# Performance work log

Measured on AMD Instinct MI355X. Metric: run time of the kernel, lower is better.

## Reference

```python
import math
import jax, jax.numpy as jnp
from jax import lax
import numpy as np

D_MODEL = 2048
N_HEADS = 16
HEAD_DIM = 128
INNER = N_HEADS * HEAD_DIM  # 2048
KCONV = 4
B, N = 2, 2048


def setup_inputs() -> dict:
    key = jax.random.key(0)
    ks = jax.random.split(key, 7)
    x = jax.random.normal(ks[0], (B, N, D_MODEL), dtype=jnp.float32)
    W_qkv = jax.random.normal(ks[1], (3 * INNER, D_MODEL), dtype=jnp.float32) * 0.02
    conv_w = jax.random.normal(ks[2], (3 * INNER, KCONV), dtype=jnp.float32) * 0.2
    W_ab = jax.random.normal(ks[3], (2 * N_HEADS, D_MODEL), dtype=jnp.float32) * 0.02
    # ab_proj bias init: first H filled with log(0.98/0.02), rest zero
    b_ab = jnp.concatenate([
        jnp.full((N_HEADS,), math.log(0.98 / 0.02), dtype=jnp.float32),
        jnp.zeros((N_HEADS,), dtype=jnp.float32),
    ])
    W_g = jax.random.normal(ks[4], (INNER, D_MODEL), dtype=jnp.float32) * 0.02
    W_o = jax.random.normal(ks[5], (D_MODEL, INNER), dtype=jnp.float32) * 0.02
    return {"x": x, "W_qkv": W_qkv, "conv_w": conv_w, "W_ab": W_ab,
            "b_ab": b_ab, "W_g": W_g, "W_o": W_o}


def _l2_normalize(t, eps=1e-12):
    # torch F.normalize: x / max(||x||_2, eps)
    nrm = jnp.sqrt(jnp.sum(t * t, axis=-1, keepdims=True))
    return t / jnp.maximum(nrm, eps)


def _short_conv(z, conv_w):
    # depthwise causal conv1d + SiLU (FLA-style ShortConvolution, no bias)
    # z: (B, N, C), conv_w: (C, K)
    C, K = conv_w.shape
    zc = jnp.transpose(z, (0, 2, 1))  # (B, C, N)
    kern = conv_w[:, None, :]          # (C, 1, K) -> OIH
    out = lax.conv_general_dilated(
        zc, kern, window_strides=(1,), padding=[(K - 1, 0)],
        dimension_numbers=("NCH", "OIH", "NCH"), feature_group_count=C)
    return jax.nn.silu(jnp.transpose(out, (0, 2, 1)))  # (B, N, C)


def reference(x, W_qkv, conv_w, W_ab, b_ab, W_g, W_o):
    Bq, Nq, _ = x.shape
    H = b_ab.shape[0] // 2
    inner = W_g.shape[0]
    D = inner // H

    qkv = jnp.einsum("bnd,ed->bne", x, W_qkv)            # (B, N, 3*inner)
    qkv = _short_conv(qkv, conv_w)
    q, k, v = jnp.split(qkv, 3, axis=-1)
    to_heads = lambda t: t.reshape(Bq, Nq, H, D).transpose(0, 2, 1, 3)  # (B,H,N,D)
    q, k, v = to_heads(q), to_heads(k), to_heads(v)
    q = _l2_normalize(q)
    k = _l2_normalize(k)

    ab = jnp.einsum("bnd,ed->bne", x, W_ab) + b_ab        # (B, N, 2H)
    alpha = jax.nn.sigmoid(ab[..., :H]).transpose(0, 2, 1)  # (B, H, N)
    beta = jax.nn.sigmoid(ab[..., H:]).transpose(0, 2, 1)   # (B, H, N)

    # gated delta rule recurrence:
    #   S_t = a_t * S_{t-1} + b_t * (v_t - a_t * S_{t-1} k_t) k_t^T
    #   o_t = S_t q_t
    # time-major xs for scan
    q_s = q.transpose(2, 0, 1, 3)   # (N, B, H, D)
    k_s = k.transpose(2, 0, 1, 3)
    v_s = v.transpose(2, 0, 1, 3)
    a_s = alpha.transpose(2, 0, 1)  # (N, B, H)
    b_s = beta.transpose(2, 0, 1)

    S0 = jnp.zeros((Bq, H, D, D), dtype=x.dtype)

    def step(S, inp):
        q_t, k_t, v_t, a_t, b_t = inp
        Sk = jnp.einsum("bhde,bhe->bhd", S, k_t)
        u = b_t[..., None] * (v_t - a_t[..., None] * Sk)
        S = a_t[..., None, None] * S + u[..., :, None] * k_t[..., None, :]
        o = jnp.einsum("bhde,bhe->bhd", S, q_t)
        return S, o

    _, o = lax.scan(step, S0, (q_s, k_s, v_s, a_s, b_s))  # o: (N, B, H, D)
    out = o.transpose(1, 0, 2, 3).reshape(Bq, Nq, inner)

    g = jax.nn.silu(jnp.einsum("bnd,ed->bne", x, W_g))
    out = out * g
    y = jnp.einsum("bne,de->bnd", out, W_o)
    return y
```

## Files before the change

### kernel.cpp

```cpp
#include <hip/hip_runtime.h>
#include <math.h>
#include <stddef.h>

#define B_ 2
#define N_ 2048
#define DM 2048
#define H_ 16
#define HD 128
#define INNER 2048
#define TRIPLE 6144
#define M_ (B_ * N_)
#define T_ 32
#define NCHK (N_ / T_)

typedef __bf16 bf16x8 __attribute__((ext_vector_type(8)));
typedef float  f32x4v __attribute__((ext_vector_type(4)));
typedef __attribute__((address_space(1))) const void gvoid;
typedef __attribute__((address_space(3))) void lvoid;

__device__ __forceinline__ float sig_(float x) { return 1.0f / (1.0f + __expf(-x)); }

__device__ __forceinline__ unsigned short f2bf(float f) {
    unsigned u = __float_as_uint(f);
    u += 0x7FFFu + ((u >> 16) & 1u);
    return (unsigned short)(u >> 16);
}
__device__ __forceinline__ float bf2f(unsigned short h) {
    return __uint_as_float((unsigned)h << 16);
}
__device__ __forceinline__ void unpack8(uint4 r, float* f) {
    f[0] = __uint_as_float(r.x << 16); f[1] = __uint_as_float(r.x & 0xffff0000u);
    f[2] = __uint_as_float(r.y << 16); f[3] = __uint_as_float(r.y & 0xffff0000u);
    f[4] = __uint_as_float(r.z << 16); f[5] = __uint_as_float(r.z & 0xffff0000u);
    f[6] = __uint_as_float(r.w << 16); f[7] = __uint_as_float(r.w & 0xffff0000u);
}

__device__ __forceinline__ void lds_barrier() {
    asm volatile("" ::: "memory");
    __builtin_amdgcn_s_waitcnt(0xC07F);
    __builtin_amdgcn_s_barrier();
    asm volatile("" ::: "memory");
}

__device__ __forceinline__ void bar() {
    asm volatile("" ::: "memory");
    __builtin_amdgcn_s_barrier();
    asm volatile("" ::: "memory");
}

__global__ __launch_bounds__(256) void cast_bf16(
    const float* __restrict__ in, unsigned short* __restrict__ out, int n)
{
    int i = (blockIdx.x * 256 + threadIdx.x) * 4;
    if (i < n) {
        float4 v = *(const float4*)(in + i);
        out[i + 0] = f2bf(v.x); out[i + 1] = f2bf(v.y);
        out[i + 2] = f2bf(v.z); out[i + 3] = f2bf(v.w);
    }
}

__global__ __launch_bounds__(256) void cast_hilo(
    const float* __restrict__ in, unsigned short* __restrict__ hi,
    unsigned short* __restrict__ lo, int n)
{
    int i = (blockIdx.x * 256 + threadIdx.x) * 4;
    if (i < n) {
        float4 v = *(const float4*)(in + i);
        ushort4 h, l;
        h.x = f2bf(v.x); l.x = f2bf(v.x - bf2f(h.x));
        h.y = f2bf(v.y); l.y = f2bf(v.y - bf2f(h.y));
        h.z = f2bf(v.z); l.z = f2bf(v.z - bf2f(h.z));
        h.w = f2bf(v.w); l.w = f2bf(v.w - bf2f(h.w));
        *(ushort4*)(hi + i) = h;
        *(ushort4*)(lo + i) = l;
    }
}

__global__ __launch_bounds__(512) void gemm_fused256(
    const unsigned short* __restrict__ A, const unsigned short* __restrict__ Bw,
    unsigned short* __restrict__ outQ, float* __restrict__ outG,
    int M, int NQ, int NG, int K)
{
    __shared__ unsigned short As[2][256 * 64];
    __shared__ unsigned short Bs[2][256 * 64];

    const int tid = threadIdx.x;
    const int w   = tid >> 6;
    const int l   = tid & 63;
    const int wm  = w >> 2;
    const int wn  = w & 3;
    const int lr  = l & 15;
    const int kg  = l >> 4;

    const int bid = blockIdx.x;
    const int swz = (bid & 7) * 64 + (bid >> 3);
    const int by  = swz & 15;
    const int bx  = swz >> 4;
    const int row0 = by * 256;
    const int col0 = bx * 256;

    const int srow = w * 8 + (l >> 3);
    const int schk = ((l & 7) ^ (l >> 3)) * 8;
    const unsigned short* Ath = A  + (size_t)(row0 + srow) * K + schk;
    const unsigned short* Bth = Bw + (size_t)(col0 + srow) * K + schk;

    const int fsw0 = ((0 + kg) ^ (lr & 7)) * 8;
    const int fsw1 = ((4 + kg) ^ (lr & 7)) * 8;
    const int arb  = wm * 64 + lr;
    const int brb  = wn * 32 + lr;

    f32x4v acc[2][2][4][2];
#pragma unroll
    for (int a0 = 0; a0 < 2; ++a0)
#pragma unroll
        for (int a1 = 0; a1 < 2; ++a1)
#pragma unroll
            for (int a2 = 0; a2 < 4; ++a2)
#pragma unroll
                for (int a3 = 0; a3 < 2; ++a3)
                    acc[a0][a1][a2][a3] = (f32x4v){0.f, 0.f, 0.f, 0.f};

#define STAGE_A(b, hb, kt) do {                                                  \
        const unsigned short* g_ = Ath + (size_t)((hb) * 128) * K + (kt) * 64;   \
        unsigned short* d_ = &As[b][((hb) * 128 + w * 8) * 64];                  \
        __builtin_amdgcn_global_load_lds((gvoid*)g_, (lvoid*)d_, 16, 0, 0);      \
        __builtin_amdgcn_global_load_lds((gvoid*)(g_ + (size_t)64 * K),          \
                                         (lvoid*)(d_ + 64 * 64), 16, 0, 0);      \
    } while (0)
#define STAGE_B(b, hb, kt) do {                                                  \
        const unsigned short* g_ = Bth + (size_t)((hb) * 128) * K + (kt) * 64;   \
        unsigned short* d_ = &Bs[b][((hb) * 128 + w * 8) * 64];                  \
        __builtin_amdgcn_global_load_lds((gvoid*)g_, (lvoid*)d_, 16, 0, 0);      \
        __builtin_amdgcn_global_load_lds((gvoid*)(g_ + (size_t)64 * K),          \
                                         (lvoid*)(d_ + 64 * 64), 16, 0, 0);      \
    } while (0)

#define RD_A(DST, BASE, HOFF)                                        \
    _Pragma("unroll")                                                \
    for (int m_ = 0; m_ < 4; ++m_) {                                 \
        const int r_ = ((HOFF) + arb + m_ * 16) * 64;                \
        DST[m_][0] = *(const bf16x8*)((BASE) + r_ + fsw0);           \
        DST[m_][1] = *(const bf16x8*)((BASE) + r_ + fsw1);           \
    }
#define RD_B(DST, BASE, HOFF)                                        \
    _Pragma("unroll")                                                \
    for (int n_ = 0; n_ < 2; ++n_) {                                 \
        const int r_ = ((HOFF) + brb + n_ * 16) * 64;                \
        DST[n_][0] = *(const bf16x8*)((BASE) + r_ + fsw0);           \
        DST[n_][1] = *(const bf16x8*)((BASE) + r_ + fsw1);           \
    }
#define Q_MFMA(MH, NH, AF, BF)                                               \
    __builtin_amdgcn_s_setprio(1);                                           \
    _Pragma("unroll")                                                        \
    for (int m_ = 0; m_ < 4; ++m_)                                           \
        _Pragma("unroll")                                                    \
        for (int n_ = 0; n_ < 2; ++n_) {                                     \
            acc[MH][NH][m_][n_] = __builtin_amdgcn_mfma_f32_16x16x32_bf16(   \
                AF[m_][0], BF[n_][0], acc[MH][NH][m_][n_], 0, 0, 0);         \
            acc[MH][NH][m_][n_] = __builtin_amdgcn_mfma_f32_16x16x32_bf16(   \
                AF[m_][1], BF[n_][1], acc[MH][NH][m_][n_], 0, 0, 0);         \
        }                                                                    \
    __builtin_amdgcn_s_setprio(0);

    const int KT = K >> 6;

    STAGE_A(0, 0, 0); STAGE_B(0, 0, 0); STAGE_A(0, 1, 0); STAGE_B(0, 1, 0);
    STAGE_A(1, 0, 1); STAGE_B(1, 1, 1);
    asm volatile("s_waitcnt vmcnt(4)" ::: "memory");
    bar();

    bf16x8 aF[4][2];
    bf16x8 aG[4][2];
    bf16x8 bF0[2][2];
    bf16x8 bF1[2][2];

#pragma unroll 2
    for (int kt = 0; kt < KT; ++kt) {
        const unsigned short* Ab = As[kt & 1];
        const unsigned short* Bb = Bs[kt & 1];
        const int nb = (kt + 1) & 1;

        RD_A(aF, Ab, 0);
        RD_B(bF0, Bb, 0);
        if (kt + 1 < KT) STAGE_B(nb, 0, kt + 1);
        bar();

        Q_MFMA(0, 0, aF, bF0);
        RD_B(bF1, Bb, 128);
        if (kt + 1 < KT) STAGE_A(nb, 1, kt + 1);
        bar();

        Q_MFMA(0, 1, aF, bF1);
        RD_A(aG, Ab, 128);
        if (kt + 2 < KT) STAGE_A(kt & 1, 0, kt + 2);
        bar();

        Q_MFMA(1, 1, aG, bF1);
        if (kt + 2 < KT) STAGE_B(kt & 1, 1, kt + 2);
        if (kt < KT - 2)       { asm volatile("s_waitcnt vmcnt(4)" ::: "memory"); }
        else if (kt == KT - 2) { asm volatile("s_waitcnt vmcnt(0)" ::: "memory"); }
        bar();
        Q_MFMA(1, 0, aG, bF0);
    }
#undef STAGE_A
#undef STAGE_B
#undef RD_A
#undef RD_B
#undef Q_MFMA

    const bool isG = (col0 >= NQ);
#pragma unroll
    for (int mh = 0; mh < 2; ++mh)
#pragma unroll
    for (int m = 0; m < 4; ++m) {
        const int rbase = row0 + mh * 128 + wm * 64 + m * 16 + kg * 4;
#pragma unroll
        for (int nh = 0; nh < 2; ++nh)
#pragma unroll
        for (int n = 0; n < 2; ++n) {
            const int c = col0 + nh * 128 + wn * 32 + n * 16 + lr;
#pragma unroll
            for (int j = 0; j < 4; ++j) {
                float v = acc[mh][nh][m][n][j];
                const size_t r = (size_t)(rbase + j);
                if (!isG) {
                    outQ[r * NQ + c] = f2bf(v);
                } else {
                    v = v * sig_(v);
                    outG[r * NG + (c - NQ)] = v;
                }
            }
        }
    }
}

__global__ __launch_bounds__(256) void gemm_bf16f(
    const unsigned short* __restrict__ A, const unsigned short* __restrict__ Bw,
    float* __restrict__ C, int M, int N, int K)
{
    __shared__ unsigned short As[128 * 32];
    __shared__ unsigned short Bs[128 * 32];
    const int tid  = threadIdx.x;
    const int w    = tid >> 6;
    const int l    = tid & 63;
    const int row0 = blockIdx.y * 128;
    const int col0 = blockIdx.x * 128;

    const int sr = tid >> 2;
    const int sc = (tid & 3) * 8;
    const unsigned short* Ag0 = A  + (size_t)(row0 + sr) * K + sc;
    const unsigned short* Ag1 = A  + (size_t)(row0 + 64 + sr) * K + sc;
    const unsigned short* Bg0 = Bw + (size_t)(col0 + sr) * K + sc;
    const unsigned short* Bg1 = Bw + (size_t)(col0 + 64 + sr) * K + sc;
    unsigned short* AsW0 = As + w * 512;
    unsigned short* AsW1 = As + 2048 + w * 512;
    unsigned short* BsW0 = Bs + w * 512;
    unsigned short* BsW1 = Bs + 2048 + w * 512;

    f32x4v acc[4][4];
#pragma unroll
    for (int i = 0; i < 4; ++i)
#pragma unroll
        for (int j = 0; j < 4; ++j) acc[i][j] = (f32x4v){0.f, 0.f, 0.f, 0.f};

    const int m0 = (w >> 1) * 64;
    const int n0 = (w & 1) * 64;
    const int lr = l & 15;
    const int lk = (l >> 4) * 8;

    for (int k0 = 0; k0 < K; k0 += 32) {
        __syncthreads();
        __builtin_amdgcn_global_load_lds((gvoid*)(Ag0 + k0), (lvoid*)AsW0, 16, 0, 0);
        __builtin_amdgcn_global_load_lds((gvoid*)(Ag1 + k0), (lvoid*)AsW1, 16, 0, 0);
        __builtin_amdgcn_global_load_lds((gvoid*)(Bg0 + k0), (lvoid*)BsW0, 16, 0, 0);
        __builtin_amdgcn_global_load_lds((gvoid*)(Bg1 + k0), (lvoid*)BsW1, 16, 0, 0);
        __syncthreads();

        bf16x8 af[4], bfr[4];
#pragma unroll
        for (int i = 0; i < 4; ++i) {
            af[i]  = *(const bf16x8*)&As[(m0 + i * 16 + lr) * 32 + lk];
            bfr[i] = *(const bf16x8*)&Bs[(n0 + i * 16 + lr) * 32 + lk];
        }
#pragma unroll
        for (int mi = 0; mi < 4; ++mi)
#pragma unroll
            for (int ni = 0; ni < 4; ++ni)
                acc[mi][ni] = __builtin_amdgcn_mfma_f32_16x16x32_bf16(
                    af[mi], bfr[ni], acc[mi][ni], 0, 0, 0);
    }

#pragma unroll
    for (int mi = 0; mi < 4; ++mi)
#pragma unroll
        for (int j = 0; j < 4; ++j) {
            int r = row0 + m0 + mi * 16 + (l >> 4) * 4 + j;
#pragma unroll
            for (int ni = 0; ni < 4; ++ni) {
                int c = col0 + n0 + ni * 16 + lr;
                C[(size_t)r * N + c] = acc[mi][ni][j];
            }
        }
}

__global__ __launch_bounds__(256) void gemm_ab(
    const unsigned short* __restrict__ xhi, const unsigned short* __restrict__ xlo,
    const unsigned short* __restrict__ wh, const unsigned short* __restrict__ wl,
    const float* __restrict__ b_ab, float* __restrict__ absig)
{
    __shared__ float sums[4][16][32];
    const int tid = threadIdx.x;
    const int w = tid >> 6, lane = tid & 63;
    const int lr = lane & 15, lk8 = (lane >> 4) * 8, lrow4 = (lane >> 4) * 4;
    const int row = blockIdx.x * 16 + lr;
    const int kw  = w * (DM / 4);

    f32x4v acc[2];
    acc[0] = (f32x4v){0.f,0.f,0.f,0.f};
    acc[1] = (f32x4v){0.f,0.f,0.f,0.f};
    const unsigned short* Ah = xhi + (size_t)row * DM + kw;
    const unsigned short* Al = xlo + (size_t)row * DM + kw;

    for (int k0 = 0; k0 < DM / 4; k0 += 32) {
        bf16x8 ah = *(const bf16x8*)(Ah + k0 + lk8);
        bf16x8 al = *(const bf16x8*)(Al + k0 + lk8);
#pragma unroll
        for (int nt = 0; nt < 2; ++nt) {
            bf16x8 whf = *(const bf16x8*)(wh + (size_t)(nt * 16 + lr) * DM + kw + k0 + lk8);
            bf16x8 wlf = *(const bf16x8*)(wl + (size_t)(nt * 16 + lr) * DM + kw + k0 + lk8);
            acc[nt] = __builtin_amdgcn_mfma_f32_16x16x32_bf16(ah, whf, acc[nt], 0, 0, 0);
            acc[nt] = __builtin_amdgcn_mfma_f32_16x16x32_bf16(ah, wlf, acc[nt], 0, 0, 0);
            acc[nt] = __builtin_amdgcn_mfma_f32_16x16x32_bf16(al, whf, acc[nt], 0, 0, 0);
        }
    }

#pragma unroll
    for (int nt = 0; nt < 2; ++nt)
#pragma unroll
        for (int j = 0; j < 4; ++j)
            sums[w][lrow4 + j][nt * 16 + lr] = acc[nt][j];
    __syncthreads();

    for (int e = tid; e < 512; e += 256) {
        const int r = e >> 5, c = e & 31;
        float s = sums[0][r][c] + sums[1][r][c] + sums[2][r][c] + sums[3][r][c];
        absig[(size_t)(blockIdx.x * 16 + r) * 32 + c] = sig_(s + b_ab[c]);
    }
}

__global__ __launch_bounds__(256) void conv_silu_norm(
    const unsigned short* __restrict__ qkv, const float* __restrict__ conv_w,
    unsigned short* __restrict__ outb)
{
    __shared__ float buf[TRIPLE];
    __shared__ float scales[32];
    const int bn = blockIdx.x;
    const int n = bn & (N_ - 1);
    const int tid = threadIdx.x;
    const unsigned short* base = qkv + (size_t)bn * TRIPLE;

#pragma unroll
    for (int it = 0; it < 3; ++it) {
        const int c8 = (tid + it * 256) * 8;
        float cw[32];
#pragma unroll
        for (int q4 = 0; q4 < 8; ++q4)
            *(float4*)&cw[q4 * 4] = *(const float4*)(conv_w + (size_t)c8 * 4 + q4 * 4);
        float acc[8] = {0.f,0.f,0.f,0.f,0.f,0.f,0.f,0.f};
#pragma unroll
        for (int j = 0; j < 4; ++j) {
            if (n - 3 + j >= 0) {
                uint4 r = *(const uint4*)(base + (ptrdiff_t)(j - 3) * TRIPLE + c8);
                float xf[8]; unpack8(r, xf);
#pragma unroll
                for (int e = 0; e < 8; ++e) acc[e] += xf[e] * cw[e * 4 + j];
            }
        }
        float4 o0, o1;
        o0.x = acc[0] * sig_(acc[0]); o0.y = acc[1] * sig_(acc[1]);
        o0.z = acc[2] * sig_(acc[2]); o0.w = acc[3] * sig_(acc[3]);
        o1.x = acc[4] * sig_(acc[4]); o1.y = acc[5] * sig_(acc[5]);
        o1.z = acc[6] * sig_(acc[6]); o1.w = acc[7] * sig_(acc[7]);
        *(float4*)&buf[c8] = o0;
        *(float4*)&buf[c8 + 4] = o1;
    }
    __syncthreads();

    const int g = tid >> 3, l = tid & 7;
    {
        int off = (g < 16) ? g * HD : 2048 + (g - 16) * HD;
        float s = 0.f;
        for (int i = l; i < HD; i += 8) { float v = buf[off + i]; s += v * v; }
        s += __shfl_xor(s, 1); s += __shfl_xor(s, 2); s += __shfl_xor(s, 4);
        if (l == 0) scales[g] = 1.0f / fmaxf(sqrtf(s), 1e-12f);
    }
    __syncthreads();

    unsigned short* ob = outb + (size_t)bn * TRIPLE;
#pragma unroll
    for (int it = 0; it < 3; ++it) {
        const int c8 = (tid + it * 256) * 8;
        float sc = 1.f;
        if (c8 < 2048) sc = scales[c8 >> 7];
        else if (c8 < 4096) sc = scales[16 + ((c8 - 2048) >> 7)];
        float4 f0 = *(const float4*)&buf[c8];
        float4 f1 = *(const float4*)&buf[c8 + 4];
        ushort4 u0, u1;
        u0.x = f2bf(f0.x * sc); u0.y = f2bf(f0.y * sc);
        u0.z = f2bf(f0.z * sc); u0.w = f2bf(f0.w * sc);
        u1.x = f2bf(f1.x * sc); u1.y = f2bf(f1.y * sc);
        u1.z = f2bf(f1.z * sc); u1.w = f2bf(f1.w * sc);
        *(ushort4*)(ob + c8) = u0;
        *(ushort4*)(ob + c8 + 4) = u1;
    }
}

__global__ __launch_bounds__(256) void chunk_prep(
    const unsigned short* __restrict__ qkvc, const float* __restrict__ absig,
    float* __restrict__ Ubar, unsigned short* __restrict__ What,
    unsigned short* __restrict__ Mhat, unsigned short* __restrict__ KhatT,
    float* __restrict__ Pbuf)
{
    __shared__ float G[T_], Pl[T_], Bl[T_];
    __shared__ float L[T_][T_ + 1];
    __shared__ float X[T_][161];
    const int bh = blockIdx.x >> 6;
    const int c  = blockIdx.x & 63;
    const int b  = bh >> 4;
    const int h  = bh & 15;
    const int tid = threadIdx.x;
    const int tok0 = c * T_;
    const size_t qbase = (size_t)b * N_ * TRIPLE;
    const unsigned short* Kb = qkvc + qbase + 2048 + h * HD;
    const unsigned short* Qb = qkvc + qbase + h * HD;
    const unsigned short* Vb = qkvc + qbase + 4096 + h * HD;
    const float* abb = absig + (size_t)b * N_ * 32;

    if (tid < T_) {
        G[tid]  = __logf(abb[(tok0 + tid) * 32 + h]);
        Bl[tid] = abb[(tok0 + tid) * 32 + 16 + h];
    }
    __syncthreads();
    if (tid == 0) {
        float run = 0.f;
        for (int t = 0; t < T_; ++t) { run += G[t]; G[t] = run; Pl[t] = __expf(run); }
    }
    __syncthreads();
    if (tid < T_) Pbuf[((size_t)bh * NCHK + c) * T_ + tid] = Pl[tid];

    const int w = tid >> 6, lane = tid & 63;
    const int lr = lane & 15, lk8 = (lane >> 4) * 8, lrow4 = (lane >> 4) * 4;
    const int mt = w >> 1, nt = w & 1;

    f32x4v akk = {0.f,0.f,0.f,0.f}, aqk = {0.f,0.f,0.f,0.f};
    const unsigned short* Km = Kb + (size_t)(tok0 + mt * 16 + lr) * TRIPLE;
    const unsigned short* Qm = Qb + (size_t)(tok0 + mt * 16 + lr) * TRIPLE;
    const unsigned short* Kn = Kb + (size_t)(tok0 + nt * 16 + lr) * TRIPLE;
#pragma unroll
    for (int ks = 0; ks < 4; ++ks) {
        bf16x8 aK = *(const bf16x8*)(Km + ks * 32 + lk8);
        bf16x8 aQ = *(const bf16x8*)(Qm + ks * 32 + lk8);
        bf16x8 bK = *(const bf16x8*)(Kn + ks * 32 + lk8);
        akk = __builtin_amdgcn_mfma_f32_16x16x32_bf16(aK, bK, akk, 0, 0, 0);
        aqk = __builtin_amdgcn_mfma_f32_16x16x32_bf16(aQ, bK, aqk, 0, 0, 0);
    }
    unsigned short* Mg = Mhat + ((size_t)bh * NCHK + c) * (T_ * T_);
#pragma unroll
    for (int reg = 0; reg < 4; ++reg) {
        int t = mt * 16 + lrow4 + reg;
        int i = nt * 16 + lr;
        float dec = __expf(G[t] - G[i]);
        L[t][i] = (i < t) ? Bl[t] * dec * akk[reg] : 0.f;
        Mg[t * T_ + i] = (i <= t) ? f2bf(dec * aqk[reg]) : (unsigned short)0;
    }
    __syncthreads();

    for (int idx = tid; idx < T_ * HD; idx += 256) {
        int t = idx >> 7, e = idx & 127;
        X[t][e] = Bl[t] * bf2f(Vb[(size_t)(tok0 + t) * TRIPLE + e]);
    }
    for (int idx = tid; idx < T_ * T_; idx += 256) {
        int t = idx >> 5, i = idx & 31;
        X[t][HD + i] = (i == t) ? Bl[t] * Pl[t] : 0.f;
    }
    __syncthreads();

    if (tid < HD + T_) {
        float x[T_];
#pragma unroll
        for (int t = 0; t < T_; ++t) x[t] = X[t][tid];
#pragma unroll
        for (int t = 1; t < T_; ++t)
#pragma unroll
            for (int i = 0; i < t; ++i)
                x[t] -= L[t][i] * x[i];
        if (tid < HD) {
            float* Ug = Ubar + ((size_t)bh * NCHK + c) * (T_ * HD);
#pragma unroll
            for (int t = 0; t < T_; ++t) Ug[t * HD + tid] = x[t];
        } else {
            unsigned short* Wg = What + ((size_t)bh * NCHK + c) * (T_ * T_);
#pragma unroll
            for (int t = 0; t < T_; ++t) Wg[t * T_ + (tid - HD)] = f2bf(x[t]);
        }
    }

    unsigned short* Kg = KhatT + ((size_t)bh * NCHK + c) * (HD * T_);
    for (int idx = tid; idx < HD * T_; idx += 256) {
        int e = idx >> 5, t = idx & 31;
        float v = __expf(G[T_ - 1] - G[t]) * bf2f(Kb[(size_t)(tok0 + t) * TRIPLE + e]);
        Kg[idx] = f2bf(v);
    }
}

__global__ __launch_bounds__(256) void chunk_scan(
    const unsigned short* __restrict__ qkvc, const float* __restrict__ gpre,
    const float* __restrict__ Ubar, const unsigned short* __restrict__ What,
    const unsigned short* __restrict__ Mhat, const unsigned short* __restrict__ KhatT,
    const float* __restrict__ Pbuf, unsigned short* __restrict__ og)
{
    __shared__ float          S  [16 * 132];
    __shared__ unsigned short Shi[16 * 136];
    __shared__ unsigned short Slo[16 * 136];
    __shared__ unsigned short CT [16 * 40];
    __shared__ unsigned short UT [16 * 40];

    const int blk = blockIdx.x;
    const int bh  = blk & 31;
    const int dsl = blk >> 5;
    const int b = bh >> 4, h = bh & 15;
    const int d0 = dsl * 16;
    const int tid = threadIdx.x;
    const int w = tid >> 6, lane = tid & 63;
    const int lr = lane & 15, lk8 = (lane >> 4) * 8, lrow4 = (lane >> 4) * 4;
    const int mt = w >> 1;
    const bool isQ = (w & 1);

    for (int i = tid; i < 16 * 132; i += 256) S[i] = 0.f;
    for (int i = tid; i < 16 * 136; i += 256) { Shi[i] = 0; Slo[i] = 0; }

    const size_t qbase = (size_t)b * N_ * TRIPLE;
    const unsigned short* Ab = qkvc + qbase + (isQ ? 0 : 2048) + h * HD;
    const float* gb = gpre + (size_t)b * N_ * INNER + h * HD;
    unsigned short* ogb = og + (size_t)b * N_ * INNER + h * HD;

    bf16x8 aF[4];
    bf16x8 wmF;
    float  sc4[4];
    float  g4[4];
    bf16x8 khF[2];
    float  gam;
    {
        const size_t cb = (size_t)bh * NCHK;
        const unsigned short* Am = Ab + (size_t)(mt * 16 + lr) * TRIPLE;
#pragma unroll
        for (int ks = 0; ks < 4; ++ks) aF[ks] = *(const bf16x8*)(Am + ks * 32 + lk8);
        if (!isQ) {
            wmF = *(const bf16x8*)(What + cb * (T_*T_) + (mt * 16 + lr) * T_ + lk8);
#pragma unroll
            for (int j = 0; j < 4; ++j)
                sc4[j] = Ubar[cb * (T_*HD) + (mt * 16 + lrow4 + j) * HD + d0 + lr];
        } else {
            wmF = *(const bf16x8*)(Mhat + cb * (T_*T_) + (mt * 16 + lr) * T_ + lk8);
#pragma unroll
            for (int j = 0; j < 4; ++j) {
                sc4[j] = Pbuf[cb * T_ + mt * 16 + lrow4 + j];
                g4[j]  = gb[(size_t)(mt * 16 + lrow4 + j) * INNER + d0 + lr];
            }
        }
#pragma unroll
        for (int j2 = 0; j2 < 2; ++j2)
            khF[j2] = *(const bf16x8*)(KhatT + cb * (HD*T_) + ((2*w + j2) * 16 + lr) * T_ + lk8);
        gam = Pbuf[cb * T_ + T_ - 1];
    }
    __syncthreads();

    for (int c = 0; c < NCHK; ++c) {
        const int np = (c + 1 < NCHK) ? c + 1 : c;
        const size_t cbn = (size_t)bh * NCHK + np;
        const int tok0n = np * T_;
        bf16x8 aFn[4], wmFn, khFn[2];
        float sc4n[4], g4n[4], gamn;
        {
            const unsigned short* Am = Ab + (size_t)(tok0n + mt * 16 + lr) * TRIPLE;
#pragma unroll
            for (int ks = 0; ks < 4; ++ks) aFn[ks] = *(const bf16x8*)(Am + ks * 32 + lk8);
            if (!isQ) {
                wmFn = *(const bf16x8*)(What + cbn * (T_*T_) + (mt * 16 + lr) * T_ + lk8);
#pragma unroll
                for (int j = 0; j < 4; ++j)
                    sc4n[j] = Ubar[cbn * (T_*HD) + (mt * 16 + lrow4 + j) * HD + d0 + lr];
            } else {
                wmFn = *(const bf16x8*)(Mhat + cbn * (T_*T_) + (mt * 16 + lr) * T_ + lk8);
#pragma unroll
                for (int j = 0; j < 4; ++j) {
                    sc4n[j] = Pbuf[cbn * T_ + mt * 16 + lrow4 + j];
                    g4n[j]  = gb[(size_t)(tok0n + mt * 16 + lrow4 + j) * INNER + d0 + lr];
                }
            }
#pragma unroll
            for (int j2 = 0; j2 < 2; ++j2)
                khFn[j2] = *(const bf16x8*)(KhatT + cbn * (HD*T_) + ((2*w + j2) * 16 + lr) * T_ + lk8);
            gamn = Pbuf[cbn * T_ + T_ - 1];
        }

        f32x4v accH = {0.f,0.f,0.f,0.f}, accL = {0.f,0.f,0.f,0.f};
#pragma unroll
        for (int ks = 0; ks < 4; ++ks) {
            bf16x8 hi = *(const bf16x8*)&Shi[lr * 136 + ks * 32 + lk8];
            bf16x8 lo = *(const bf16x8*)&Slo[lr * 136 + ks * 32 + lk8];
            accH = __builtin_amdgcn_mfma_f32_16x16x32_bf16(aF[ks], hi, accH, 0, 0, 0);
            accL = __builtin_amdgcn_mfma_f32_16x16x32_bf16(aF[ks], lo, accL, 0, 0, 0);
        }
        f32x4v accB;
#pragma unroll
        for (int j = 0; j < 4; ++j) accB[j] = accH[j] + accL[j];

        if (!isQ) {
            ushort4 cv;
            cv.x = f2bf(-accB[0]); cv.y = f2bf(-accB[1]);
            cv.z = f2bf(-accB[2]); cv.w = f2bf(-accB[3]);
            *(ushort4*)&CT[lr * 40 + mt * 16 + lrow4] = cv;
        }
        lds_barrier();

        if (!isQ) {
            f32x4v accU;
#pragma unroll
            for (int j = 0; j < 4; ++j) accU[j] = sc4[j];
            bf16x8 bC = *(const bf16x8*)&CT[lr * 40 + lk8];
            accU = __builtin_amdgcn_mfma_f32_16x16x32_bf16(wmF, bC, accU, 0, 0, 0);
            ushort4 uv;
            uv.x = f2bf(accU[0]); uv.y = f2bf(accU[1]);
            uv.z = f2bf(accU[2]); uv.w = f2bf(accU[3]);
            *(ushort4*)&UT[lr * 40 + mt * 16 + lrow4] = uv;
        }
        lds_barrier();

        bf16x8 utF = *(const bf16x8*)&UT[lr * 40 + lk8];

        if (isQ) {
            f32x4v accO;
#pragma unroll
            for (int j = 0; j < 4; ++j) accO[j] = sc4[j] * accB[j];
            accO = __builtin_amdgcn_mfma_f32_16x16x32_bf16(wmF, utF, accO, 0, 0, 0);
            const int tokb = c * T_ + mt * 16 + lrow4;
#pragma unroll
            for (int j = 0; j < 4; ++j)
                ogb[(size_t)(tokb + j) * INNER + d0 + lr] = f2bf(accO[j] * g4[j]);
        }

#pragma unroll
        for (int j2 = 0; j2 < 2; ++j2) {
            const int et = 2 * w + j2;
            f32x4v accS;
#pragma unroll
            for (int j = 0; j < 4; ++j)
                accS[j] = gam * S[(lrow4 + j) * 132 + et * 16 + lr];
            accS = __builtin_amdgcn_mfma_f32_16x16x32_bf16(utF, khF[j2], accS, 0, 0, 0);
#pragma unroll
            for (int j = 0; j < 4; ++j) {
                float v = accS[j];
                S[(lrow4 + j) * 132 + et * 16 + lr] = v;
                unsigned short hh = f2bf(v);
                Shi[(lrow4 + j) * 136 + et * 16 + lr] = hh;
                Slo[(lrow4 + j) * 136 + et * 16 + lr] = f2bf(v - bf2f(hh));
            }
        }
        lds_barrier();

#pragma unroll
        for (int ks = 0; ks < 4; ++ks) aF[ks] = aFn[ks];
        wmF = wmFn;
#pragma unroll
        for (int j = 0; j < 4; ++j) { sc4[j] = sc4n[j]; g4[j] = g4n[j]; }
        khF[0] = khFn[0]; khF[1] = khFn[1];
        gam = gamn;
    }
}

extern "C" void kernel_launch(void* const* d_in, const int* in_sizes, int n_in,
                              void* d_out, int out_size, void* d_ws, size_t ws_size,
                              hipStream_t stream) {
    const float* x      = (const float*)d_in[0];
    const float* W_qkv  = (const float*)d_in[1];
    const float* conv_w = (const float*)d_in[2];
    const float* W_ab   = (const float*)d_in[3];
    const float* b_ab   = (const float*)d_in[4];
    const float* W_g    = (const float*)d_in[5];
    const float* W_o    = (const float*)d_in[6];
    float* out = (float*)d_out;

    char* p = (char*)d_ws;
    unsigned short* wqkvb   = (unsigned short*)p; p += (size_t)TRIPLE * DM * 2;
    unsigned short* wgb     = (unsigned short*)p; p += (size_t)INNER * DM * 2;
    unsigned short* wob     = (unsigned short*)p; p += (size_t)DM * INNER * 2;
    unsigned short* wabhi   = (unsigned short*)p; p += (size_t)32 * DM * 2;
    unsigned short* wablo   = (unsigned short*)p; p += (size_t)32 * DM * 2;
    unsigned short* xb      = (unsigned short*)p; p += (size_t)M_ * DM * 2;
    unsigned short* xlo     = (unsigned short*)p; p += (size_t)M_ * DM * 2;
    unsigned short* qkv_pre = (unsigned short*)p; p += (size_t)M_ * TRIPLE * 2;
    unsigned short* qkv_c   = (unsigned short*)p; p += (size_t)M_ * TRIPLE * 2;
    float*          absig   = (float*)p;          p += (size_t)M_ * 32 * 4;
    float*          gpre    = (float*)p;          p += (size_t)M_ * INNER * 4;
    unsigned short* ogb     = (unsigned short*)p; p += (size_t)M_ * INNER * 2;

    char* q = (char*)xb;
    float*          Ubar  = (float*)q;          q += (size_t)32 * NCHK * T_ * HD * 4;
    unsigned short* KhatT = (unsigned short*)q; q += (size_t)32 * NCHK * HD * T_ * 2;
    unsigned short* What  = (unsigned short*)q; q += (size_t)32 * NCHK * T_ * T_ * 2;
    unsigned short* Mhat  = (unsigned short*)q; q += (size_t)32 * NCHK * T_ * T_ * 2;
    float*          Pbuf  = (float*)q;          q += (size_t)32 * NCHK * T_ * 4;

    dim3 blk(256);
    cast_hilo<<<dim3((M_ * DM) / 1024), blk, 0, stream>>>(x, xb, xlo, M_ * DM);
    cast_bf16<<<dim3((TRIPLE * DM) / 1024), blk, 0, stream>>>(W_qkv, wqkvb, TRIPLE * DM);
    cast_bf16<<<dim3((INNER * DM) / 1024), blk, 0, stream>>>(W_g, wgb, INNER * DM);
    cast_bf16<<<dim3((INNER * DM) / 1024), blk, 0, stream>>>(W_o, wob, INNER * DM);
    cast_hilo<<<dim3((32 * DM) / 1024), blk, 0, stream>>>(W_ab, wabhi, wablo, 32 * DM);

    gemm_fused256<<<dim3(((TRIPLE + INNER) / 256) * (M_ / 256)), dim3(512), 0, stream>>>(
        xb, wqkvb, qkv_pre, gpre, M_, TRIPLE, INNER, DM);
    gemm_ab<<<dim3(M_ / 16), blk, 0, stream>>>(xb, xlo, wabhi, wablo, b_ab, absig);
    conv_silu_norm<<<dim3(B_ * N_), blk, 0, stream>>>(qkv_pre, conv_w, qkv_c);

    chunk_prep<<<dim3(32 * NCHK), blk, 0, stream>>>(qkv_c, absig, Ubar, What, Mhat, KhatT, Pbuf);
    chunk_scan<<<dim3(256), blk, 0, stream>>>(qkv_c, gpre, Ubar, What, Mhat, KhatT, Pbuf, ogb);

    gemm_bf16f<<<dim3(INNER / 128, M_ / 128), blk, 0, stream>>>(ogb, wob, out, M_, INNER, DM);
}
```

Baseline: 595.3 us.

## Prefetch next-tile LDS fragments across MFMA phases and fuse weight casts

Restructures the fused GEMM mainloop so the A/B register fragments for the next k-tile are read from LDS while the current tile's MFMAs run, with the global-to-LDS staging order reshuffled to match. MFMA issue order becomes k-outer. The three bf16 weight cast launches are merged into one kernel writing a contiguous destination. This adds register pressure and depends on wqkvb/wgb/wob being laid out contiguously.

```diff
diff --git a/kernel.cpp b/kernel.cpp
--- a/kernel.cpp
+++ b/kernel.cpp
@@ -57,6 +57,23 @@
         out[i + 0] = f2bf(v.x); out[i + 1] = f2bf(v.y);
         out[i + 2] = f2bf(v.z); out[i + 3] = f2bf(v.w);
     }
+}
+
+__global__ __launch_bounds__(256) void cast_bf16_3(
+    const float* __restrict__ s1, const float* __restrict__ s2,
+    const float* __restrict__ s3, unsigned short* __restrict__ dst,
+    int n1, int n2, int n3)
+{
+    int i = (blockIdx.x * 256 + threadIdx.x) * 4;
+    const float* s; int off;
+    if (i < n1)           { s = s1; off = i; }
+    else if (i < n1 + n2) { s = s2; off = i - n1; }
+    else if (i < n1 + n2 + n3) { s = s3; off = i - n1 - n2; }
+    else return;
+    float4 v = *(const float4*)(s + off);
+    ushort4 u;
+    u.x = f2bf(v.x); u.y = f2bf(v.y); u.z = f2bf(v.z); u.w = f2bf(v.w);
+    *(ushort4*)(dst + i) = u;
 }
 
 __global__ __launch_bounds__(256) void cast_hilo(
@@ -135,13 +152,11 @@
                                          (lvoid*)(d_ + 64 * 64), 16, 0, 0);      \
     } while (0)
 
-#define RD_A(DST, BASE, HOFF)                                        \
-    _Pragma("unroll")                                                \
-    for (int m_ = 0; m_ < 4; ++m_) {                                 \
-        const int r_ = ((HOFF) + arb + m_ * 16) * 64;                \
-        DST[m_][0] = *(const bf16x8*)((BASE) + r_ + fsw0);           \
-        DST[m_][1] = *(const bf16x8*)((BASE) + r_ + fsw1);           \
-    }
+#define RD_A1(DST, M_IDX, BASE, HOFF) do {                           \
+        const int r_ = ((HOFF) + arb + (M_IDX) * 16) * 64;           \
+        DST[M_IDX][0] = *(const bf16x8*)((BASE) + r_ + fsw0);        \
+        DST[M_IDX][1] = *(const bf16x8*)((BASE) + r_ + fsw1);        \
+    } while (0)
 #define RD_B(DST, BASE, HOFF)                                        \
     _Pragma("unroll")                                                \
     for (int n_ = 0; n_ < 2; ++n_) {                                 \
@@ -152,20 +167,19 @@
 #define Q_MFMA(MH, NH, AF, BF)                                               \
     __builtin_amdgcn_s_setprio(1);                                           \
     _Pragma("unroll")                                                        \
-    for (int m_ = 0; m_ < 4; ++m_)                                           \
+    for (int k_ = 0; k_ < 2; ++k_)                                           \
         _Pragma("unroll")                                                    \
-        for (int n_ = 0; n_ < 2; ++n_) {                                     \
-            acc[MH][NH][m_][n_] = __builtin_amdgcn_mfma_f32_16x16x32_bf16(   \
-                AF[m_][0], BF[n_][0], acc[MH][NH][m_][n_], 0, 0, 0);         \
-            acc[MH][NH][m_][n_] = __builtin_amdgcn_mfma_f32_16x16x32_bf16(   \
-                AF[m_][1], BF[n_][1], acc[MH][NH][m_][n_], 0, 0, 0);         \
-        }                                                                    \
+        for (int m_ = 0; m_ < 4; ++m_)                                       \
+            _Pragma("unroll")                                                \
+            for (int n_ = 0; n_ < 2; ++n_)                                   \
+                acc[MH][NH][m_][n_] = __builtin_amdgcn_mfma_f32_16x16x32_bf16(\
+                    AF[m_][k_], BF[n_][k_], acc[MH][NH][m_][n_], 0, 0, 0);   \
     __builtin_amdgcn_s_setprio(0);
 
     const int KT = K >> 6;
 
     STAGE_A(0, 0, 0); STAGE_B(0, 0, 0); STAGE_A(0, 1, 0); STAGE_B(0, 1, 0);
-    STAGE_A(1, 0, 1); STAGE_B(1, 1, 1);
+    STAGE_A(1, 0, 1); STAGE_B(1, 0, 1);
     asm volatile("s_waitcnt vmcnt(4)" ::: "memory");
     bar();
 
@@ -174,37 +188,60 @@
     bf16x8 bF0[2][2];
     bf16x8 bF1[2][2];
 
+#pragma unroll
+    for (int m_ = 0; m_ < 4; ++m_) RD_A1(aF, m_, As[0], 0);
+    RD_B(bF0, Bs[0], 0);
+
 #pragma unroll 2
     for (int kt = 0; kt < KT; ++kt) {
         const unsigned short* Ab = As[kt & 1];
         const unsigned short* Bb = Bs[kt & 1];
+        const unsigned short* An = As[(kt + 1) & 1];
+        const unsigned short* Bn = Bs[(kt + 1) & 1];
         const int nb = (kt + 1) & 1;
-
-        RD_A(aF, Ab, 0);
-        RD_B(bF0, Bb, 0);
-        if (kt + 1 < KT) STAGE_B(nb, 0, kt + 1);
-        bar();
+        const int cb = kt & 1;
 
         Q_MFMA(0, 0, aF, bF0);
         RD_B(bF1, Bb, 128);
+        RD_A1(aG, 0, Ab, 128);
         if (kt + 1 < KT) STAGE_A(nb, 1, kt + 1);
         bar();
 
         Q_MFMA(0, 1, aF, bF1);
-        RD_A(aG, Ab, 128);
-        if (kt + 2 < KT) STAGE_A(kt & 1, 0, kt + 2);
+        RD_A1(aG, 1, Ab, 128);
+        RD_A1(aG, 2, Ab, 128);
+        RD_A1(aG, 3, Ab, 128);
+        if (kt + 1 < KT) {
+            STAGE_B(nb, 1, kt + 1);
+            asm volatile("s_waitcnt vmcnt(4)" ::: "memory");
+        }
         bar();
 
         Q_MFMA(1, 1, aG, bF1);
-        if (kt + 2 < KT) STAGE_B(kt & 1, 1, kt + 2);
-        if (kt < KT - 2)       { asm volatile("s_waitcnt vmcnt(4)" ::: "memory"); }
-        else if (kt == KT - 2) { asm volatile("s_waitcnt vmcnt(0)" ::: "memory"); }
+        if (kt + 1 < KT) {
+            RD_A1(aF, 0, An, 0);
+            RD_A1(aF, 1, An, 0);
+            RD_A1(aF, 2, An, 0);
+        }
+        if (kt + 2 < KT) STAGE_A(cb, 0, kt + 2);
         bar();
+
         Q_MFMA(1, 0, aG, bF0);
+        if (kt + 1 < KT) {
+            RD_A1(aF, 3, An, 0);
+            RD_B(bF0, Bn, 0);
+        }
+        if (kt + 2 < KT) STAGE_B(cb, 0, kt + 2);
+        if (kt < KT - 2) {
+            asm volatile("s_waitcnt vmcnt(4)" ::: "memory");
+        } else if (kt == KT - 2) {
+            asm volatile("s_waitcnt vmcnt(0)" ::: "memory");
+        }
+        bar();
     }
 #undef STAGE_A
 #undef STAGE_B
-#undef RD_A
+#undef RD_A1
 #undef RD_B
 #undef Q_MFMA
 
@@ -714,9 +751,8 @@
 
     dim3 blk(256);
     cast_hilo<<<dim3((M_ * DM) / 1024), blk, 0, stream>>>(x, xb, xlo, M_ * DM);
-    cast_bf16<<<dim3((TRIPLE * DM) / 1024), blk, 0, stream>>>(W_qkv, wqkvb, TRIPLE * DM);
-    cast_bf16<<<dim3((INNER * DM) / 1024), blk, 0, stream>>>(W_g, wgb, INNER * DM);
-    cast_bf16<<<dim3((INNER * DM) / 1024), blk, 0, stream>>>(W_o, wob, INNER * DM);
+    cast_bf16_3<<<dim3((TRIPLE * DM + INNER * DM + DM * INNER) / 1024), blk, 0, stream>>>(
+        W_qkv, W_g, W_o, wqkvb, TRIPLE * DM, INNER * DM, DM * INNER);
     cast_hilo<<<dim3((32 * DM) / 1024), blk, 0, stream>>>(W_ab, wabhi, wablo, 32 * DM);
 
     gemm_fused256<<<dim3(((TRIPLE + INNER) / 256) * (M_ / 256)), dim3(512), 0, stream>>>(
```

New measurement: 582.1 us. -2.2%, faster.

## Double-buffer output GEMM with swizzled LDS and merge weight cast kernels

Applied to the files above, without the earlier changes.

Rewrites the output-projection GEMM to use a K-tile of 64 with two LDS buffers. Global-to-LDS loads for tile k+2 are issued while MFMAs run on the current tile, and the LDS chunks are XOR-swizzled to avoid bank conflicts. A block-index swizzle is added so neighbouring blocks share operands in L2. Three separate weight cast launches are folded into one kernel with vectorized stores, which assumes the destination buffers are contiguous. The GEMM now uses 64KB of LDS per block and relies on exact vmcnt accounting.

```diff
diff --git a/kernel.cpp b/kernel.cpp
--- a/kernel.cpp
+++ b/kernel.cpp
@@ -48,15 +48,21 @@
     asm volatile("" ::: "memory");
 }
 
-__global__ __launch_bounds__(256) void cast_bf16(
-    const float* __restrict__ in, unsigned short* __restrict__ out, int n)
+__global__ __launch_bounds__(256) void cast_bf16_3(
+    const float* __restrict__ s1, const float* __restrict__ s2,
+    const float* __restrict__ s3, unsigned short* __restrict__ dst,
+    int n1, int n2, int n3)
 {
     int i = (blockIdx.x * 256 + threadIdx.x) * 4;
-    if (i < n) {
-        float4 v = *(const float4*)(in + i);
-        out[i + 0] = f2bf(v.x); out[i + 1] = f2bf(v.y);
-        out[i + 2] = f2bf(v.z); out[i + 3] = f2bf(v.w);
-    }
+    const float* s; int off;
+    if (i < n1)           { s = s1; off = i; }
+    else if (i < n1 + n2) { s = s2; off = i - n1; }
+    else if (i < n1 + n2 + n3) { s = s3; off = i - n1 - n2; }
+    else return;
+    float4 v = *(const float4*)(s + off);
+    ushort4 u;
+    u.x = f2bf(v.x); u.y = f2bf(v.y); u.z = f2bf(v.z); u.w = f2bf(v.w);
+    *(ushort4*)(dst + i) = u;
 }
 
 __global__ __launch_bounds__(256) void cast_hilo(
@@ -238,24 +244,33 @@
     const unsigned short* __restrict__ A, const unsigned short* __restrict__ Bw,
     float* __restrict__ C, int M, int N, int K)
 {
-    __shared__ unsigned short As[128 * 32];
-    __shared__ unsigned short Bs[128 * 32];
-    const int tid  = threadIdx.x;
-    const int w    = tid >> 6;
-    const int l    = tid & 63;
-    const int row0 = blockIdx.y * 128;
-    const int col0 = blockIdx.x * 128;
-
-    const int sr = tid >> 2;
-    const int sc = (tid & 3) * 8;
-    const unsigned short* Ag0 = A  + (size_t)(row0 + sr) * K + sc;
-    const unsigned short* Ag1 = A  + (size_t)(row0 + 64 + sr) * K + sc;
-    const unsigned short* Bg0 = Bw + (size_t)(col0 + sr) * K + sc;
-    const unsigned short* Bg1 = Bw + (size_t)(col0 + 64 + sr) * K + sc;
-    unsigned short* AsW0 = As + w * 512;
-    unsigned short* AsW1 = As + 2048 + w * 512;
-    unsigned short* BsW0 = Bs + w * 512;
-    unsigned short* BsW1 = Bs + 2048 + w * 512;
+    __shared__ unsigned short As[2][128 * 64];
+    __shared__ unsigned short Bs[2][128 * 64];
+
+    const int tid = threadIdx.x;
+    const int w   = tid >> 6;
+    const int l   = tid & 63;
+    const int wm  = w >> 1;
+    const int wn  = w & 1;
+    const int lr  = l & 15;
+    const int kg  = l >> 4;
+
+    const int bid = blockIdx.x;
+    const int swz = (bid & 7) * 64 + (bid >> 3);
+    const int by  = swz & 31;
+    const int bx  = swz >> 5;
+    const int row0 = by * 128;
+    const int col0 = bx * 128;
+
+    const int srow = w * 8 + (l >> 3);
+    const int schk = ((l & 7) ^ (l >> 3)) * 8;
+    const unsigned short* Ath = A  + (size_t)(row0 + srow) * K + schk;
+    const unsigned short* Bth = Bw + (size_t)(col0 + srow) * K + schk;
+
+    const int fsw0 = ((0 + kg) ^ (lr & 7)) * 8;
+    const int fsw1 = ((4 + kg) ^ (lr & 7)) * 8;
+    const int arb  = wm * 64 + lr;
+    const int brb  = wn * 64 + lr;
 
     f32x4v acc[4][4];
 #pragma unroll
@@ -263,42 +278,77 @@
 #pragma unroll
         for (int j = 0; j < 4; ++j) acc[i][j] = (f32x4v){0.f, 0.f, 0.f, 0.f};
 
-    const int m0 = (w >> 1) * 64;
-    const int n0 = (w & 1) * 64;
-    const int lr = l & 15;
-    const int lk = (l >> 4) * 8;
-
-    for (int k0 = 0; k0 < K; k0 += 32) {
-        __syncthreads();
-        __builtin_amdgcn_global_load_lds((gvoid*)(Ag0 + k0), (lvoid*)AsW0, 16, 0, 0);
-        __builtin_amdgcn_global_load_lds((gvoid*)(Ag1 + k0), (lvoid*)AsW1, 16, 0, 0);
-        __builtin_amdgcn_global_load_lds((gvoid*)(Bg0 + k0), (lvoid*)BsW0, 16, 0, 0);
-        __builtin_amdgcn_global_load_lds((gvoid*)(Bg1 + k0), (lvoid*)BsW1, 16, 0, 0);
-        __syncthreads();
-
-        bf16x8 af[4], bfr[4];
-#pragma unroll
-        for (int i = 0; i < 4; ++i) {
-            af[i]  = *(const bf16x8*)&As[(m0 + i * 16 + lr) * 32 + lk];
-            bfr[i] = *(const bf16x8*)&Bs[(n0 + i * 16 + lr) * 32 + lk];
-        }
-#pragma unroll
-        for (int mi = 0; mi < 4; ++mi)
-#pragma unroll
-            for (int ni = 0; ni < 4; ++ni)
-                acc[mi][ni] = __builtin_amdgcn_mfma_f32_16x16x32_bf16(
-                    af[mi], bfr[ni], acc[mi][ni], 0, 0, 0);
-    }
-
-#pragma unroll
-    for (int mi = 0; mi < 4; ++mi)
+#define STAGE_T(buf, kt) do {                                                    \
+        _Pragma("unroll")                                                        \
+        for (int p_ = 0; p_ < 4; ++p_) {                                         \
+            const unsigned short* ga_ = Ath + (size_t)(p_ * 32) * K + (kt) * 64; \
+            const unsigned short* gb_ = Bth + (size_t)(p_ * 32) * K + (kt) * 64; \
+            unsigned short* da_ = &As[buf][(p_ * 32 + w * 8) * 64];              \
+            unsigned short* db_ = &Bs[buf][(p_ * 32 + w * 8) * 64];              \
+            __builtin_amdgcn_global_load_lds((gvoid*)ga_, (lvoid*)da_, 16, 0, 0);\
+            __builtin_amdgcn_global_load_lds((gvoid*)gb_, (lvoid*)db_, 16, 0, 0);\
+        }                                                                        \
+    } while (0)
+
+    const int KT = K >> 6;
+
+    STAGE_T(0, 0);
+    STAGE_T(1, 1);
+    asm volatile("s_waitcnt vmcnt(8)" ::: "memory");
+    bar();
+
+    bf16x8 aF[4][2], bF[4][2];
+
+#pragma unroll 2
+    for (int kt = 0; kt < KT; ++kt) {
+        const unsigned short* Ab = As[kt & 1];
+        const unsigned short* Bb = Bs[kt & 1];
+
+#pragma unroll
+        for (int m_ = 0; m_ < 4; ++m_) {
+            const int r_ = (arb + m_ * 16) * 64;
+            aF[m_][0] = *(const bf16x8*)(Ab + r_ + fsw0);
+            aF[m_][1] = *(const bf16x8*)(Ab + r_ + fsw1);
+        }
+#pragma unroll
+        for (int n_ = 0; n_ < 4; ++n_) {
+            const int r_ = (brb + n_ * 16) * 64;
+            bF[n_][0] = *(const bf16x8*)(Bb + r_ + fsw0);
+            bF[n_][1] = *(const bf16x8*)(Bb + r_ + fsw1);
+        }
+        bar();
+
+        if (kt + 2 < KT) STAGE_T(kt & 1, kt + 2);
+
+        __builtin_amdgcn_s_setprio(1);
+#pragma unroll
+        for (int ks = 0; ks < 2; ++ks)
+#pragma unroll
+            for (int m_ = 0; m_ < 4; ++m_)
+#pragma unroll
+                for (int n_ = 0; n_ < 4; ++n_)
+                    acc[m_][n_] = __builtin_amdgcn_mfma_f32_16x16x32_bf16(
+                        aF[m_][ks], bF[n_][ks], acc[m_][n_], 0, 0, 0);
+        __builtin_amdgcn_s_setprio(0);
+
+        if (kt < KT - 2) {
+            asm volatile("s_waitcnt vmcnt(8)" ::: "memory");
+        } else if (kt == KT - 2) {
+            asm volatile("s_waitcnt vmcnt(0)" ::: "memory");
+        }
+        bar();
+    }
+#undef STAGE_T
+
+#pragma unroll
+    for (int m_ = 0; m_ < 4; ++m_)
 #pragma unroll
         for (int j = 0; j < 4; ++j) {
-            int r = row0 + m0 + mi * 16 + (l >> 4) * 4 + j;
-#pragma unroll
-            for (int ni = 0; ni < 4; ++ni) {
-                int c = col0 + n0 + ni * 16 + lr;
-                C[(size_t)r * N + c] = acc[mi][ni][j];
+            const int r = row0 + wm * 64 + m_ * 16 + kg * 4 + j;
+#pragma unroll
+            for (int n_ = 0; n_ < 4; ++n_) {
+                const int c = col0 + wn * 64 + n_ * 16 + lr;
+                C[(size_t)r * N + c] = acc[m_][n_][j];
             }
         }
 }
@@ -714,9 +764,8 @@
 
     dim3 blk(256);
     cast_hilo<<<dim3((M_ * DM) / 1024), blk, 0, stream>>>(x, xb, xlo, M_ * DM);
-    cast_bf16<<<dim3((TRIPLE * DM) / 1024), blk, 0, stream>>>(W_qkv, wqkvb, TRIPLE * DM);
-    cast_bf16<<<dim3((INNER * DM) / 1024), blk, 0, stream>>>(W_g, wgb, INNER * DM);
-    cast_bf16<<<dim3((INNER * DM) / 1024), blk, 0, stream>>>(W_o, wob, INNER * DM);
+    cast_bf16_3<<<dim3((TRIPLE * DM + INNER * DM + DM * INNER) / 1024), blk, 0, stream>>>(
+        W_qkv, W_g, W_o, wqkvb, TRIPLE * DM, INNER * DM, DM * INNER);
     cast_hilo<<<dim3((32 * DM) / 1024), blk, 0, stream>>>(W_ab, wabhi, wablo, 32 * DM);
 
     gemm_fused256<<<dim3(((TRIPLE + INNER) / 256) * (M_ / 256)), dim3(512), 0, stream>>>(
@@ -727,5 +776,6 @@
     chunk_prep<<<dim3(32 * NCHK), blk, 0, stream>>>(qkv_c, absig, Ubar, What, Mhat, KhatT, Pbuf);
     chunk_scan<<<dim3(256), blk, 0, stream>>>(qkv_c, gpre, Ubar, What, Mhat, KhatT, Pbuf, ogb);
 
-    gemm_bf16f<<<dim3(INNER / 128, M_ / 128), blk, 0, stream>>>(ogb, wob, out, M_, INNER, DM);
-}
+    gemm_bf16f<<<dim3((M_ / 128) * (INNER / 128)), blk, 0, stream>>>(
+        ogb, wob, out, M_, INNER, DM);
+}
```

Result: faster. 556.1 us (-6.6%).
